# Kernel tuning notes

Hardware: AMD Instinct MI355X
Metric: run time of the kernel (lower is better)

## Reference

```python
import jax, jax.numpy as jnp
from jax import lax
import numpy as np

EMBED_HD = 3
DECODE_HD = 128
B, TX, TS = 256, 512, 512


def _lstm(x_seq, h0, c0, Wih, Whh, bih, bhh):
    """PyTorch-convention LSTM over time. x_seq: [T, B, D]; returns final h [B, H].
    Gate order i, f, g, o; gates = x W_ih^T + h W_hh^T + b_ih + b_hh."""
    b = bih + bhh

    def step(carry, x_t):
        h, c = carry
        gates = x_t @ Wih.T + h @ Whh.T + b  # [B, 4H]
        i, f, g, o = jnp.split(gates, 4, axis=-1)
        c = jax.nn.sigmoid(f) * c + jax.nn.sigmoid(i) * jnp.tanh(g)
        h = jax.nn.sigmoid(o) * jnp.tanh(c)
        return (h, c), None

    (hT, _cT), _ = lax.scan(step, (h0, c0), x_seq)
    return hT


def setup_inputs() -> dict:
    key = jax.random.key(0)
    ks = jax.random.split(key, 16)
    f32 = jnp.float32
    return {
        "x": jax.random.normal(ks[0], (B, TX, 8), f32),
        "s": jax.random.normal(ks[1], (B, TS, 6), f32),
        "h0": jax.random.normal(ks[2], (B, EMBED_HD), f32),
        "c0": jax.random.normal(ks[3], (B, EMBED_HD), f32),
        "We_ih": jax.random.normal(ks[4], (4 * EMBED_HD, 8), f32) * 0.1,
        "We_hh": jax.random.normal(ks[5], (4 * EMBED_HD, EMBED_HD), f32) * 0.1,
        "be_ih": jax.random.normal(ks[6], (4 * EMBED_HD,), f32) * 0.1,
        "be_hh": jax.random.normal(ks[7], (4 * EMBED_HD,), f32) * 0.1,
        "Wfc_e": jax.random.normal(ks[8], (1, EMBED_HD), f32) * 0.1,
        "bfc_e": jax.random.normal(ks[9], (1,), f32) * 0.1,
        "Wd_ih": jax.random.normal(ks[10], (4 * DECODE_HD, 7), f32) * 0.1,
        "Wd_hh": jax.random.normal(ks[11], (4 * DECODE_HD, DECODE_HD), f32) * 0.1,
        "bd_ih": jax.random.normal(ks[12], (4 * DECODE_HD,), f32) * 0.1,
        "bd_hh": jax.random.normal(ks[13], (4 * DECODE_HD,), f32) * 0.1,
        "Wfc_d": jax.random.normal(ks[14], (2, 6), f32) * 0.1,
        "bfc_d": jax.random.normal(ks[15], (2,), f32) * 0.1,
    }


def reference(x, s, h0, c0, We_ih, We_hh, be_ih, be_hh, Wfc_e, bfc_e,
              Wd_ih, Wd_hh, bd_ih, bd_hh, Wfc_d, bfc_d):
    # ---- encoder: LSTM over x, random initial hidden (h0, c0), take final out ----
    h_enc = _lstm(jnp.swapaxes(x, 0, 1), h0, c0, We_ih, We_hh, be_ih, be_hh)  # [B, 3]
    z = h_enc @ Wfc_e.T + bfc_e  # [B, 1]

    # ---- decoder: LSTM over cat(s_t, z), zero initial hidden ----
    z_seq = jnp.broadcast_to(z[:, None, :], (s.shape[0], s.shape[1], 1))
    s_plus_z = jnp.concatenate([s, z_seq], axis=-1)  # [B, T, 7]
    hz = jnp.zeros((s.shape[0], DECODE_HD), s.dtype)
    h_dec = _lstm(jnp.swapaxes(s_plus_z, 0, 1), hz, hz, Wd_ih, Wd_hh, bd_ih, bd_hh)

    # per the source, decode_fc is applied to s itself (not the LSTM output)
    traj_hat = s @ Wfc_d.T + bfc_d  # [B, T, 2]
    return z, traj_hat, h_dec
```

## Files before the change

### kernel.cpp

```cpp
#include <hip/hip_runtime.h>
#include <math.h>

#define BATCH 256
#define TX 512
#define TS 512
#define DH 128

typedef _Float16 h2 __attribute__((ext_vector_type(2)));

__device__ __forceinline__ float sigf(float x) {
    return __builtin_amdgcn_rcpf(1.0f + __expf(-x));
}
__device__ __forceinline__ float tanhfast(float x) {
    return fmaf(-2.0f, __builtin_amdgcn_rcpf(__expf(2.0f * x) + 1.0f), 1.0f);
}
template<int CTRL>
__device__ __forceinline__ float dpp_f32(float x) {
    return __int_as_float(__builtin_amdgcn_update_dpp(
        0, __float_as_int(x), CTRL, 0xF, 0xF, true));
}
#define DPP_XOR1 0xB1
#define DPP_XOR2 0x4E
#define DPP_BC0  0x00
#define DPP_BC1  0x55
#define DPP_BC2  0xAA

__global__ __launch_bounds__(512) void enc_pre_kernel(
    const float* __restrict__ x,
    const float* __restrict__ We_ih, const float* __restrict__ be_ih,
    const float* __restrict__ be_hh, float* __restrict__ pre)
{
    const int b = blockIdx.x, t = threadIdx.x;
    const float* xp = x + ((size_t)b * TX + t) * 8;
    const float4 x0 = *(const float4*)(xp);
    const float4 x1 = *(const float4*)(xp + 4);

    float o[12];
    #pragma unroll
    for (int g = 0; g < 4; ++g) {
        #pragma unroll
        for (int kk = 0; kk < 3; ++kk) {
            const int row = g * 3 + kk;
            const float* wr = We_ih + row * 8;
            float d = be_ih[row] + be_hh[row];
            d = fmaf(wr[0], x0.x, d); d = fmaf(wr[1], x0.y, d);
            d = fmaf(wr[2], x0.z, d); d = fmaf(wr[3], x0.w, d);
            d = fmaf(wr[4], x1.x, d); d = fmaf(wr[5], x1.y, d);
            d = fmaf(wr[6], x1.z, d); d = fmaf(wr[7], x1.w, d);
            o[kk * 4 + g] = d;
        }
    }
    float* op = pre + ((size_t)b * TX + t) * 12;
    *(float4*)(op)     = make_float4(o[0], o[1], o[2],  o[3]);
    *(float4*)(op + 4) = make_float4(o[4], o[5], o[6],  o[7]);
    *(float4*)(op + 8) = make_float4(o[8], o[9], o[10], o[11]);
}

__global__ __launch_bounds__(64) void enc_kernel(
    const float* __restrict__ pre, const float* __restrict__ h0,
    const float* __restrict__ c0, const float* __restrict__ We_hh,
    const float* __restrict__ Wfc_e, const float* __restrict__ bfc_e,
    float* __restrict__ out_z)
{
    const int gt = blockIdx.x * 64 + threadIdx.x;
    const int b  = gt >> 2;
    const int k  = gt & 3;
    const int kk = (k < 3) ? k : 0;

    float wh[4][3];
    #pragma unroll
    for (int g = 0; g < 4; ++g) {
        const int row = g * 3 + kk;
        #pragma unroll
        for (int n = 0; n < 3; ++n) wh[g][n] = We_hh[row * 3 + n];
    }

    float hv0 = h0[b * 3 + 0], hv1 = h0[b * 3 + 1], hv2 = h0[b * 3 + 2];
    float c = c0[b * 3 + kk];

    const float* pb = pre + (size_t)b * TX * 12 + kk * 4;
    float4 P0 = *(const float4*)(pb);
    float4 P1 = *(const float4*)(pb + 12);
    float4 P2 = *(const float4*)(pb + 24);

    for (int t = 0; t < TX; ++t) {
        const int tn = (t + 3 < TX) ? t + 3 : TX - 1;
        const float4 pn = *(const float4*)(pb + (size_t)tn * 12);

        float a0 = P0.x, a1 = P0.y, a2 = P0.z, a3 = P0.w;
        a0 = fmaf(wh[0][0], hv0, a0); a0 = fmaf(wh[0][1], hv1, a0); a0 = fmaf(wh[0][2], hv2, a0);
        a1 = fmaf(wh[1][0], hv0, a1); a1 = fmaf(wh[1][1], hv1, a1); a1 = fmaf(wh[1][2], hv2, a1);
        a2 = fmaf(wh[2][0], hv0, a2); a2 = fmaf(wh[2][1], hv1, a2); a2 = fmaf(wh[2][2], hv2, a2);
        a3 = fmaf(wh[3][0], hv0, a3); a3 = fmaf(wh[3][1], hv1, a3); a3 = fmaf(wh[3][2], hv2, a3);

        const float ig = sigf(a0);
        const float fg = sigf(a1);
        const float gg = tanhfast(a2);
        const float og = sigf(a3);
        c = fmaf(fg, c, ig * gg);
        const float hk = og * tanhfast(c);
        hv0 = dpp_f32<DPP_BC0>(hk);
        hv1 = dpp_f32<DPP_BC1>(hk);
        hv2 = dpp_f32<DPP_BC2>(hk);
        P0 = P1; P1 = P2; P2 = pn;
    }

    if (k == 0) {
        float zz = bfc_e[0];
        zz = fmaf(hv0, Wfc_e[0], zz);
        zz = fmaf(hv1, Wfc_e[1], zz);
        zz = fmaf(hv2, Wfc_e[2], zz);
        out_z[b] = zz;
    }
}

__global__ __launch_bounds__(512, 1) void dec_kernel(
    const float* __restrict__ s, const float* __restrict__ z,
    const float* __restrict__ Wd_ih, const float* __restrict__ Wd_hh,
    const float* __restrict__ bd_ih, const float* __restrict__ bd_hh,
    const float* __restrict__ Wfc_d, const float* __restrict__ bfc_d,
    float* __restrict__ out_traj, float* __restrict__ out_h)
{
    __shared__ int hbuf[2][64];

    const int b   = blockIdx.x;
    const int tid = threadIdx.x;
    const int j   = tid >> 2;
    const int q   = tid & 3;

    {
        const int t = tid;
        const float* st = s + ((size_t)b * TS + t) * 6;
        const float2 sa = *(const float2*)(st);
        const float2 sbb = *(const float2*)(st + 2);
        const float2 sc = *(const float2*)(st + 4);
        float o0 = bfc_d[0];
        o0 = fmaf(sa.x,  Wfc_d[0], o0); o0 = fmaf(sa.y,  Wfc_d[1], o0);
        o0 = fmaf(sbb.x, Wfc_d[2], o0); o0 = fmaf(sbb.y, Wfc_d[3], o0);
        o0 = fmaf(sc.x,  Wfc_d[4], o0); o0 = fmaf(sc.y,  Wfc_d[5], o0);
        float o1 = bfc_d[1];
        o1 = fmaf(sa.x,  Wfc_d[6],  o1); o1 = fmaf(sa.y,  Wfc_d[7],  o1);
        o1 = fmaf(sbb.x, Wfc_d[8],  o1); o1 = fmaf(sbb.y, Wfc_d[9],  o1);
        o1 = fmaf(sc.x,  Wfc_d[10], o1); o1 = fmaf(sc.y,  Wfc_d[11], o1);
        *(float2*)(out_traj + ((size_t)b * TS + t) * 2) = make_float2(o0, o1);
    }

    h2 w[4][16];
    #pragma unroll
    for (int g = 0; g < 4; ++g) {
        const float* wp = Wd_hh + (size_t)(g * DH + j) * DH + q * 32;
        #pragma unroll
        for (int k = 0; k < 16; ++k)
            w[g][k] = h2{(_Float16)wp[2 * k], (_Float16)wp[2 * k + 1]};
    }
    const float* wi = Wd_ih + (size_t)(q * DH + j) * 7;
    const float wx0 = wi[0], wx1 = wi[1], wx2 = wi[2];
    const float wx3 = wi[3], wx4 = wi[4], wx5 = wi[5];
    const float gb  = bd_ih[q * DH + j] + bd_hh[q * DH + j] + z[b] * wi[6];

    if (tid < 64) hbuf[0][tid] = 0;
    float c = 0.0f;
    float hn = 0.0f;
    __syncthreads();

    const float* sb = s + (size_t)b * TS * 6;
    float2 sA = *(const float2*)(sb);
    float2 sB = *(const float2*)(sb + 2);
    float2 sC = *(const float2*)(sb + 4);
    const float* sp = sb + 6;

#define DEC_STEP(T)                                                            \
    {                                                                          \
        const int4* hb = (const int4*)(&hbuf[(T) & 1][q * 16]);                \
        const int4 hA = hb[0], hB = hb[1], hC = hb[2], hD = hb[3];             \
        h2 hh[16];                                                             \
        hh[0]  = __builtin_bit_cast(h2, hA.x); hh[1]  = __builtin_bit_cast(h2, hA.y); \
        hh[2]  = __builtin_bit_cast(h2, hA.z); hh[3]  = __builtin_bit_cast(h2, hA.w); \
        hh[4]  = __builtin_bit_cast(h2, hB.x); hh[5]  = __builtin_bit_cast(h2, hB.y); \
        hh[6]  = __builtin_bit_cast(h2, hB.z); hh[7]  = __builtin_bit_cast(h2, hB.w); \
        hh[8]  = __builtin_bit_cast(h2, hC.x); hh[9]  = __builtin_bit_cast(h2, hC.y); \
        hh[10] = __builtin_bit_cast(h2, hC.z); hh[11] = __builtin_bit_cast(h2, hC.w); \
        hh[12] = __builtin_bit_cast(h2, hD.x); hh[13] = __builtin_bit_cast(h2, hD.y); \
        hh[14] = __builtin_bit_cast(h2, hD.z); hh[15] = __builtin_bit_cast(h2, hD.w); \
        float sdot = gb;                                                       \
        sdot = fmaf(wx0, sA.x, sdot);                                          \
        sdot = fmaf(wx1, sA.y, sdot);                                          \
        sdot = fmaf(wx2, sB.x, sdot);                                          \
        sdot = fmaf(wx3, sB.y, sdot);                                          \
        sdot = fmaf(wx4, sC.x, sdot);                                          \
        sdot = fmaf(wx5, sC.y, sdot);                                          \
        float acc[4];                                                          \
        _Pragma("unroll")                                                      \
        for (int g = 0; g < 4; ++g) {                                          \
            float p = (g == q) ? sdot : 0.0f;                                  \
            _Pragma("unroll")                                                  \
            for (int k = 0; k < 16; ++k)                                       \
                p = __builtin_amdgcn_fdot2(w[g][k], hh[k], p, false);          \
            acc[g] = p;                                                        \
        }                                                                      \
        _Pragma("unroll")                                                      \
        for (int g = 0; g < 4; ++g) {                                          \
            float v = acc[g];                                                  \
            v += dpp_f32<DPP_XOR1>(v);                                         \
            v += dpp_f32<DPP_XOR2>(v);                                         \
            acc[g] = v;                                                        \
        }                                                                      \
        const float ig = sigf(acc[0]);                                         \
        const float fg = sigf(acc[1]);                                         \
        const float gg = tanhfast(acc[2]);                                     \
        const float og = sigf(acc[3]);                                         \
        c  = fmaf(fg, c, ig * gg);                                             \
        hn = og * tanhfast(c);                                                 \
        if (q == 0) ((_Float16*)hbuf[((T) + 1) & 1])[j] = (_Float16)hn;        \
        __syncthreads();                                                       \
    }

    for (int t = 0; t < TS - 1; ++t) {
        const float2 nA = *(const float2*)(sp);
        const float2 nB = *(const float2*)(sp + 2);
        const float2 nC = *(const float2*)(sp + 4);
        sp += 6;
        DEC_STEP(t);
        sA = nA; sB = nB; sC = nC;
    }
    DEC_STEP(TS - 1);
#undef DEC_STEP

    if (q == 0) out_h[(size_t)b * DH + j] = hn;
}

extern "C" void kernel_launch(void* const* d_in, const int* in_sizes, int n_in,
                              void* d_out, int out_size, void* d_ws, size_t ws_size,
                              hipStream_t stream) {
    const float* x      = (const float*)d_in[0];
    const float* s      = (const float*)d_in[1];
    const float* h0     = (const float*)d_in[2];
    const float* c0     = (const float*)d_in[3];
    const float* We_ih  = (const float*)d_in[4];
    const float* We_hh  = (const float*)d_in[5];
    const float* be_ih  = (const float*)d_in[6];
    const float* be_hh  = (const float*)d_in[7];
    const float* Wfc_e  = (const float*)d_in[8];
    const float* bfc_e  = (const float*)d_in[9];
    const float* Wd_ih  = (const float*)d_in[10];
    const float* Wd_hh  = (const float*)d_in[11];
    const float* bd_ih  = (const float*)d_in[12];
    const float* bd_hh  = (const float*)d_in[13];
    const float* Wfc_d  = (const float*)d_in[14];
    const float* bfc_d  = (const float*)d_in[15];

    float* out      = (float*)d_out;
    float* out_z    = out;
    float* out_traj = out + BATCH;
    float* out_h    = out + BATCH + BATCH * TS * 2;

    float* pre = (float*)d_ws;

    enc_pre_kernel<<<BATCH, 512, 0, stream>>>(x, We_ih, be_ih, be_hh, pre);
    enc_kernel<<<16, 64, 0, stream>>>(pre, h0, c0, We_hh, Wfc_e, bfc_e, out_z);
    dec_kernel<<<BATCH, 512, 0, stream>>>(s, out_z, Wd_ih, Wd_hh, bd_ih, bd_hh,
                                          Wfc_d, bfc_d, out_traj, out_h);
}
```

Baseline: 482.5 us.

## Fuse encoder precompute, encoder recurrence and decoder into one per-batch kernel

Merges the three launches into a single kernel with one block per batch element. The encoder input projection is staged in LDS instead of a global workspace, and four threads of each block run the encoder recurrence before the decoder starts. This removes two launch boundaries and the global round trip of the precomputed gates. In exchange, every block spends the serial encoder time with 508 threads idle, and the decoder loop is unrolled by two with constant buffer indices and a deeper prefetch of s.

```diff
diff --git a/kernel.cpp b/kernel.cpp
--- a/kernel.cpp
+++ b/kernel.cpp
@@ -25,103 +25,21 @@
 #define DPP_BC1  0x55
 #define DPP_BC2  0xAA
 
-__global__ __launch_bounds__(512) void enc_pre_kernel(
-    const float* __restrict__ x,
-    const float* __restrict__ We_ih, const float* __restrict__ be_ih,
-    const float* __restrict__ be_hh, float* __restrict__ pre)
-{
-    const int b = blockIdx.x, t = threadIdx.x;
-    const float* xp = x + ((size_t)b * TX + t) * 8;
-    const float4 x0 = *(const float4*)(xp);
-    const float4 x1 = *(const float4*)(xp + 4);
-
-    float o[12];
-    #pragma unroll
-    for (int g = 0; g < 4; ++g) {
-        #pragma unroll
-        for (int kk = 0; kk < 3; ++kk) {
-            const int row = g * 3 + kk;
-            const float* wr = We_ih + row * 8;
-            float d = be_ih[row] + be_hh[row];
-            d = fmaf(wr[0], x0.x, d); d = fmaf(wr[1], x0.y, d);
-            d = fmaf(wr[2], x0.z, d); d = fmaf(wr[3], x0.w, d);
-            d = fmaf(wr[4], x1.x, d); d = fmaf(wr[5], x1.y, d);
-            d = fmaf(wr[6], x1.z, d); d = fmaf(wr[7], x1.w, d);
-            o[kk * 4 + g] = d;
-        }
-    }
-    float* op = pre + ((size_t)b * TX + t) * 12;
-    *(float4*)(op)     = make_float4(o[0], o[1], o[2],  o[3]);
-    *(float4*)(op + 4) = make_float4(o[4], o[5], o[6],  o[7]);
-    *(float4*)(op + 8) = make_float4(o[8], o[9], o[10], o[11]);
-}
-
-__global__ __launch_bounds__(64) void enc_kernel(
-    const float* __restrict__ pre, const float* __restrict__ h0,
-    const float* __restrict__ c0, const float* __restrict__ We_hh,
+__global__ __launch_bounds__(512) void fused_kernel(
+    const float* __restrict__ x, const float* __restrict__ s,
+    const float* __restrict__ h0, const float* __restrict__ c0,
+    const float* __restrict__ We_ih, const float* __restrict__ We_hh,
+    const float* __restrict__ be_ih, const float* __restrict__ be_hh,
     const float* __restrict__ Wfc_e, const float* __restrict__ bfc_e,
-    float* __restrict__ out_z)
-{
-    const int gt = blockIdx.x * 64 + threadIdx.x;
-    const int b  = gt >> 2;
-    const int k  = gt & 3;
-    const int kk = (k < 3) ? k : 0;
-
-    float wh[4][3];
-    #pragma unroll
-    for (int g = 0; g < 4; ++g) {
-        const int row = g * 3 + kk;
-        #pragma unroll
-        for (int n = 0; n < 3; ++n) wh[g][n] = We_hh[row * 3 + n];
-    }
-
-    float hv0 = h0[b * 3 + 0], hv1 = h0[b * 3 + 1], hv2 = h0[b * 3 + 2];
-    float c = c0[b * 3 + kk];
-
-    const float* pb = pre + (size_t)b * TX * 12 + kk * 4;
-    float4 P0 = *(const float4*)(pb);
-    float4 P1 = *(const float4*)(pb + 12);
-    float4 P2 = *(const float4*)(pb + 24);
-
-    for (int t = 0; t < TX; ++t) {
-        const int tn = (t + 3 < TX) ? t + 3 : TX - 1;
-        const float4 pn = *(const float4*)(pb + (size_t)tn * 12);
-
-        float a0 = P0.x, a1 = P0.y, a2 = P0.z, a3 = P0.w;
-        a0 = fmaf(wh[0][0], hv0, a0); a0 = fmaf(wh[0][1], hv1, a0); a0 = fmaf(wh[0][2], hv2, a0);
-        a1 = fmaf(wh[1][0], hv0, a1); a1 = fmaf(wh[1][1], hv1, a1); a1 = fmaf(wh[1][2], hv2, a1);
-        a2 = fmaf(wh[2][0], hv0, a2); a2 = fmaf(wh[2][1], hv1, a2); a2 = fmaf(wh[2][2], hv2, a2);
-        a3 = fmaf(wh[3][0], hv0, a3); a3 = fmaf(wh[3][1], hv1, a3); a3 = fmaf(wh[3][2], hv2, a3);
-
-        const float ig = sigf(a0);
-        const float fg = sigf(a1);
-        const float gg = tanhfast(a2);
-        const float og = sigf(a3);
-        c = fmaf(fg, c, ig * gg);
-        const float hk = og * tanhfast(c);
-        hv0 = dpp_f32<DPP_BC0>(hk);
-        hv1 = dpp_f32<DPP_BC1>(hk);
-        hv2 = dpp_f32<DPP_BC2>(hk);
-        P0 = P1; P1 = P2; P2 = pn;
-    }
-
-    if (k == 0) {
-        float zz = bfc_e[0];
-        zz = fmaf(hv0, Wfc_e[0], zz);
-        zz = fmaf(hv1, Wfc_e[1], zz);
-        zz = fmaf(hv2, Wfc_e[2], zz);
-        out_z[b] = zz;
-    }
-}
-
-__global__ __launch_bounds__(512, 1) void dec_kernel(
-    const float* __restrict__ s, const float* __restrict__ z,
     const float* __restrict__ Wd_ih, const float* __restrict__ Wd_hh,
     const float* __restrict__ bd_ih, const float* __restrict__ bd_hh,
     const float* __restrict__ Wfc_d, const float* __restrict__ bfc_d,
-    float* __restrict__ out_traj, float* __restrict__ out_h)
+    float* __restrict__ out_z, float* __restrict__ out_traj,
+    float* __restrict__ out_h)
 {
+    __shared__ __align__(16) float pre_lds[TX][12];
     __shared__ int hbuf[2][64];
+    __shared__ float zslot;
 
     const int b   = blockIdx.x;
     const int tid = threadIdx.x;
@@ -129,8 +47,33 @@
     const int q   = tid & 3;
 
     {
-        const int t = tid;
-        const float* st = s + ((size_t)b * TS + t) * 6;
+        const float* xp = x + ((size_t)b * TX + tid) * 8;
+        const float4 x0 = *(const float4*)(xp);
+        const float4 x1 = *(const float4*)(xp + 4);
+        float o[12];
+        #pragma unroll
+        for (int g = 0; g < 4; ++g) {
+            #pragma unroll
+            for (int kk = 0; kk < 3; ++kk) {
+                const int row = g * 3 + kk;
+                const float* wr = We_ih + row * 8;
+                float d = be_ih[row] + be_hh[row];
+                d = fmaf(wr[0], x0.x, d); d = fmaf(wr[1], x0.y, d);
+                d = fmaf(wr[2], x0.z, d); d = fmaf(wr[3], x0.w, d);
+                d = fmaf(wr[4], x1.x, d); d = fmaf(wr[5], x1.y, d);
+                d = fmaf(wr[6], x1.z, d); d = fmaf(wr[7], x1.w, d);
+                o[kk * 4 + g] = d;
+            }
+        }
+        float* op = pre_lds[tid];
+        *(float4*)(op)     = make_float4(o[0], o[1], o[2],  o[3]);
+        *(float4*)(op + 4) = make_float4(o[4], o[5], o[6],  o[7]);
+        *(float4*)(op + 8) = make_float4(o[8], o[9], o[10], o[11]);
+    }
+    if (tid < 64) hbuf[0][tid] = 0;
+
+    {
+        const float* st = s + ((size_t)b * TS + tid) * 6;
         const float2 sa = *(const float2*)(st);
         const float2 sbb = *(const float2*)(st + 2);
         const float2 sc = *(const float2*)(st + 4);
@@ -142,7 +85,7 @@
         o1 = fmaf(sa.x,  Wfc_d[6],  o1); o1 = fmaf(sa.y,  Wfc_d[7],  o1);
         o1 = fmaf(sbb.x, Wfc_d[8],  o1); o1 = fmaf(sbb.y, Wfc_d[9],  o1);
         o1 = fmaf(sc.x,  Wfc_d[10], o1); o1 = fmaf(sc.y,  Wfc_d[11], o1);
-        *(float2*)(out_traj + ((size_t)b * TS + t) * 2) = make_float2(o0, o1);
+        *(float2*)(out_traj + ((size_t)b * TS + tid) * 2) = make_float2(o0, o1);
     }
 
     h2 w[4][16];
@@ -156,23 +99,80 @@
     const float* wi = Wd_ih + (size_t)(q * DH + j) * 7;
     const float wx0 = wi[0], wx1 = wi[1], wx2 = wi[2];
     const float wx3 = wi[3], wx4 = wi[4], wx5 = wi[5];
-    const float gb  = bd_ih[q * DH + j] + bd_hh[q * DH + j] + z[b] * wi[6];
-
-    if (tid < 64) hbuf[0][tid] = 0;
+    const float bsum = bd_ih[q * DH + j] + bd_hh[q * DH + j];
+    const float wz = wi[6];
+
+    __syncthreads();
+
+    if (tid < 4) {
+        const int kk = (tid < 3) ? tid : 0;
+        float wh[4][3];
+        #pragma unroll
+        for (int g = 0; g < 4; ++g) {
+            const int row = g * 3 + kk;
+            #pragma unroll
+            for (int n = 0; n < 3; ++n) wh[g][n] = We_hh[row * 3 + n];
+        }
+        float hv0 = h0[b * 3 + 0], hv1 = h0[b * 3 + 1], hv2 = h0[b * 3 + 2];
+        float c = c0[b * 3 + kk];
+
+        float4 P = *(const float4*)(&pre_lds[0][kk * 4]);
+        for (int t = 0; t < TX; ++t) {
+            const int tn = (t + 1 < TX) ? t + 1 : t;
+            const float4 Pn = *(const float4*)(&pre_lds[tn][kk * 4]);
+
+            float a0 = P.x, a1 = P.y, a2 = P.z, a3 = P.w;
+            a0 = fmaf(wh[0][0], hv0, a0); a0 = fmaf(wh[0][1], hv1, a0); a0 = fmaf(wh[0][2], hv2, a0);
+            a1 = fmaf(wh[1][0], hv0, a1); a1 = fmaf(wh[1][1], hv1, a1); a1 = fmaf(wh[1][2], hv2, a1);
+            a2 = fmaf(wh[2][0], hv0, a2); a2 = fmaf(wh[2][1], hv1, a2); a2 = fmaf(wh[2][2], hv2, a2);
+            a3 = fmaf(wh[3][0], hv0, a3); a3 = fmaf(wh[3][1], hv1, a3); a3 = fmaf(wh[3][2], hv2, a3);
+
+            const float ig = sigf(a0);
+            const float fg = sigf(a1);
+            const float gg = tanhfast(a2);
+            const float og = sigf(a3);
+            c = fmaf(fg, c, ig * gg);
+            const float hk = og * tanhfast(c);
+            hv0 = dpp_f32<DPP_BC0>(hk);
+            hv1 = dpp_f32<DPP_BC1>(hk);
+            hv2 = dpp_f32<DPP_BC2>(hk);
+            P = Pn;
+        }
+        if (tid == 0) {
+            float zz = bfc_e[0];
+            zz = fmaf(hv0, Wfc_e[0], zz);
+            zz = fmaf(hv1, Wfc_e[1], zz);
+            zz = fmaf(hv2, Wfc_e[2], zz);
+            zslot = zz;
+            out_z[b] = zz;
+        }
+    }
+    __syncthreads();
+
+    const float gb = bsum + zslot * wz;
+
     float c = 0.0f;
     float hn = 0.0f;
-    __syncthreads();
 
     const float* sb = s + (size_t)b * TS * 6;
     float2 sA = *(const float2*)(sb);
     float2 sB = *(const float2*)(sb + 2);
     float2 sC = *(const float2*)(sb + 4);
-    const float* sp = sb + 6;
-
-#define DEC_STEP(T)                                                            \
+    float2 sD = *(const float2*)(sb + 6);
+    float2 sE = *(const float2*)(sb + 8);
+    float2 sF = *(const float2*)(sb + 10);
+
+#define DEC_STEP(BUF, XA, XB, XC)                                              \
     {                                                                          \
-        const int4* hb = (const int4*)(&hbuf[(T) & 1][q * 16]);                \
+        const int4* hb = (const int4*)(&hbuf[BUF][q * 16]);                    \
         const int4 hA = hb[0], hB = hb[1], hC = hb[2], hD = hb[3];             \
+        float sdot = gb;                                                       \
+        sdot = fmaf(wx0, XA.x, sdot);                                          \
+        sdot = fmaf(wx1, XA.y, sdot);                                          \
+        sdot = fmaf(wx2, XB.x, sdot);                                          \
+        sdot = fmaf(wx3, XB.y, sdot);                                          \
+        sdot = fmaf(wx4, XC.x, sdot);                                          \
+        sdot = fmaf(wx5, XC.y, sdot);                                          \
         h2 hh[16];                                                             \
         hh[0]  = __builtin_bit_cast(h2, hA.x); hh[1]  = __builtin_bit_cast(h2, hA.y); \
         hh[2]  = __builtin_bit_cast(h2, hA.z); hh[3]  = __builtin_bit_cast(h2, hA.w); \
@@ -182,13 +182,6 @@
         hh[10] = __builtin_bit_cast(h2, hC.z); hh[11] = __builtin_bit_cast(h2, hC.w); \
         hh[12] = __builtin_bit_cast(h2, hD.x); hh[13] = __builtin_bit_cast(h2, hD.y); \
         hh[14] = __builtin_bit_cast(h2, hD.z); hh[15] = __builtin_bit_cast(h2, hD.w); \
-        float sdot = gb;                                                       \
-        sdot = fmaf(wx0, sA.x, sdot);                                          \
-        sdot = fmaf(wx1, sA.y, sdot);                                          \
-        sdot = fmaf(wx2, sB.x, sdot);                                          \
-        sdot = fmaf(wx3, sB.y, sdot);                                          \
-        sdot = fmaf(wx4, sC.x, sdot);                                          \
-        sdot = fmaf(wx5, sC.y, sdot);                                          \
         float acc[4];                                                          \
         _Pragma("unroll")                                                      \
         for (int g = 0; g < 4; ++g) {                                          \
@@ -211,19 +204,28 @@
         const float og = sigf(acc[3]);                                         \
         c  = fmaf(fg, c, ig * gg);                                             \
         hn = og * tanhfast(c);                                                 \
-        if (q == 0) ((_Float16*)hbuf[((T) + 1) & 1])[j] = (_Float16)hn;        \
+        if (q == 0) ((_Float16*)hbuf[BUF ^ 1])[j] = (_Float16)hn;              \
         __syncthreads();                                                       \
     }
 
-    for (int t = 0; t < TS - 1; ++t) {
-        const float2 nA = *(const float2*)(sp);
-        const float2 nB = *(const float2*)(sp + 2);
-        const float2 nC = *(const float2*)(sp + 4);
-        sp += 6;
-        DEC_STEP(t);
-        sA = nA; sB = nB; sC = nC;
-    }
-    DEC_STEP(TS - 1);
+    for (int t = 0; t < TS; t += 2) {
+        DEC_STEP(0, sA, sB, sC);
+        {
+            const int tn = (t + 2 < TS) ? t + 2 : TS - 1;
+            const float* p = sb + (size_t)tn * 6;
+            sA = *(const float2*)(p);
+            sB = *(const float2*)(p + 2);
+            sC = *(const float2*)(p + 4);
+        }
+        DEC_STEP(1, sD, sE, sF);
+        {
+            const int tn = (t + 3 < TS) ? t + 3 : TS - 1;
+            const float* p = sb + (size_t)tn * 6;
+            sD = *(const float2*)(p);
+            sE = *(const float2*)(p + 2);
+            sF = *(const float2*)(p + 4);
+        }
+    }
 #undef DEC_STEP
 
     if (q == 0) out_h[(size_t)b * DH + j] = hn;
@@ -254,10 +256,8 @@
     float* out_traj = out + BATCH;
     float* out_h    = out + BATCH + BATCH * TS * 2;
 
-    float* pre = (float*)d_ws;
-
-    enc_pre_kernel<<<BATCH, 512, 0, stream>>>(x, We_ih, be_ih, be_hh, pre);
-    enc_kernel<<<16, 64, 0, stream>>>(pre, h0, c0, We_hh, Wfc_e, bfc_e, out_z);
-    dec_kernel<<<BATCH, 512, 0, stream>>>(s, out_z, Wd_ih, Wd_hh, bd_ih, bd_hh,
-                                          Wfc_d, bfc_d, out_traj, out_h);
-}
+    fused_kernel<<<BATCH, 512, 0, stream>>>(
+        x, s, h0, c0, We_ih, We_hh, be_ih, be_hh, Wfc_e, bfc_e,
+        Wd_ih, Wd_hh, bd_ih, bd_hh, Wfc_d, bfc_d,
+        out_z, out_traj, out_h);
+}
```

Measured after the change: 452.6 us. 6.2% less time.
